# Optimization experiments

Hardware: AMD Instinct MI355X
Metric: run time of the kernel (lower is better)

The kernel has to match this reference:

```python
import jax, jax.numpy as jnp
import numpy as np

EPS = 1e-5
GRID = 128          # coarse grid extent -> fine grid is 256^3
N1 = 15000          # coarse voxels
CHILD = 4           # children kept per coarse voxel
N2 = N1 * CHILD     # fine voxels
CIN = 128
COUT = 64


def _build_geometry():
    rng = np.random.RandomState(0)
    flat = rng.choice(GRID ** 3, N1, replace=False)
    cc = np.stack(np.unravel_index(flat, (GRID, GRID, GRID)), axis=1)  # [N1,3]
    offs8 = np.array([[i, j, k] for i in (0, 1) for j in (0, 1) for k in (0, 1)], dtype=np.int64)
    kidx = np.argsort(rng.rand(N1, 8), axis=1)[:, :CHILD]              # [N1,4] distinct child taps
    fine = (cc[:, None, :] * 2 + offs8[kidx]).reshape(-1, 3)           # [N2,3] unique fine coords
    up_src = np.repeat(np.arange(N1), CHILD).astype(np.int32)
    up_kidx = kidx.reshape(-1).astype(np.int32)
    # 27-offset neighbor maps via hashed coordinate lookup
    key = (fine[:, 0] * 256 + fine[:, 1]) * 256 + fine[:, 2]
    order = np.argsort(key)
    skey = key[order]
    offs27 = np.array([[i, j, k] for i in (-1, 0, 1) for j in (-1, 0, 1) for k in (-1, 0, 1)], dtype=np.int64)
    nbr_src = np.full((27, N2), N2, dtype=np.int32)
    nbr_dst = np.full((27, N2), N2, dtype=np.int32)
    for t in range(27):
        q = fine + offs27[t]
        inb = np.all((q >= 0) & (q < 256), axis=1)
        qk = (q[:, 0] * 256 + q[:, 1]) * 256 + q[:, 2]
        pos = np.searchsorted(skey, qk)
        pos = np.clip(pos, 0, N2 - 1)
        hit = inb & (skey[pos] == qk)
        nbr_src[t, hit] = order[pos[hit]]
        nbr_dst[t, hit] = np.arange(N2, dtype=np.int32)[hit]
    return up_src, up_kidx, nbr_src, nbr_dst


def setup_inputs() -> dict:
    key = jax.random.key(0)
    ks = jax.random.split(key, 8)
    up_src, up_kidx, nbr_src, nbr_dst = _build_geometry()
    s_up = 1.0 / np.sqrt(CIN * 8)
    s1 = 1.0 / np.sqrt(CIN * 27)
    s2 = 1.0 / np.sqrt(COUT * 27)
    return {
        "feats1": jax.random.normal(ks[0], (N1, CIN), jnp.float32),
        "feats2": jax.random.normal(ks[1], (N2, CIN // 2), jnp.float32),
        "w_up": jax.random.normal(ks[2], (8, CIN, CIN // 2), jnp.float32) * s_up,
        "gamma_up": jnp.ones((CIN // 2,), jnp.float32),
        "beta_up": jnp.zeros((CIN // 2,), jnp.float32),
        "w1": jax.random.normal(ks[3], (27, CIN, COUT), jnp.float32) * s1,
        "gamma1": jnp.ones((COUT,), jnp.float32),
        "beta1": jnp.zeros((COUT,), jnp.float32),
        "w2": jax.random.normal(ks[4], (27, COUT, COUT), jnp.float32) * s2,
        "gamma2": jnp.ones((COUT,), jnp.float32),
        "beta2": jnp.zeros((COUT,), jnp.float32),
        "up_src": jnp.asarray(up_src),
        "up_kidx": jnp.asarray(up_kidx),
        "nbr_src": jnp.asarray(nbr_src),
        "nbr_dst": jnp.asarray(nbr_dst),
    }


def _bn_relu(x, gamma, beta):
    # training-mode BatchNorm over the point dimension (biased variance), then ReLU
    m = jnp.mean(x, axis=0)
    v = jnp.var(x, axis=0)
    return jax.nn.relu((x - m) * jax.lax.rsqrt(v + EPS) * gamma + beta)


def _sparse_conv(x, w, nbr_src, nbr_dst):
    # x: [N,Ci]; w: [27,Ci,Co]; transform-then-gather-scatter (hash-map sparse conv)
    n = x.shape[0]
    co = w.shape[-1]
    y = jnp.einsum("nc,kco->kno", x, w)                       # [27,N,Co]
    y = jnp.concatenate([y, jnp.zeros((27, 1, co), y.dtype)], axis=1)  # sentinel row
    msg = jnp.take_along_axis(y, nbr_src[:, :, None], axis=1)  # [27,N,Co]
    out = jnp.zeros((n + 1, co), y.dtype).at[nbr_dst.reshape(-1)].add(msg.reshape(-1, co))
    return out[:-1]


def reference(feats1, feats2, w_up, gamma_up, beta_up, w1, gamma1, beta1, w2,
              gamma2, beta2, up_src, up_kidx, nbr_src, nbr_dst):
    # transposed conv k=2 s=2, generative=False: each fine voxel pulls from its unique coarse parent
    y = jnp.einsum("mc,kco->kmo", feats1, w_up)               # [8,N1,Cin/2]
    x1 = y[up_kidx, up_src]                                   # [N2,Cin/2]
    x1 = _bn_relu(x1, gamma_up, beta_up)
    x = jnp.concatenate([x1, feats2], axis=-1)                # [N2,Cin]
    h = _bn_relu(_sparse_conv(x, w1, nbr_src, nbr_dst), gamma1, beta1)
    return _bn_relu(_sparse_conv(h, w2, nbr_src, nbr_dst), gamma2, beta2)
```

## Files before the change

kernel.cpp:

```cpp
#include <hip/hip_runtime.h>


typedef short bf16x4 __attribute__((ext_vector_type(4)));
typedef short bf16x8 __attribute__((ext_vector_type(8)));
typedef float f32x16 __attribute__((ext_vector_type(16)));

__device__ __forceinline__ short f2bf(float f) {
    unsigned u = __float_as_uint(f);
    u += 0x7fffu + ((u >> 16) & 1u);
    return (short)(u >> 16);
}
__device__ __forceinline__ float bf2f(short s) {
    return __uint_as_float(((unsigned)(unsigned short)s) << 16);
}

__global__ __launch_bounds__(256) void k_setup(
    const float* __restrict__ w_up, const float* __restrict__ w1,
    const float* __restrict__ w2, const float* __restrict__ f1,
    const int* __restrict__ nbr, const int* __restrict__ up_kidx,
    short* __restrict__ wupp, short* __restrict__ w1p,
    short* __restrict__ w2p, short* __restrict__ f1bf,
    int* __restrict__ pmask, int* __restrict__ perm_rows,
    int* __restrict__ rank, int* __restrict__ cnt,
    int2* __restrict__ ext, int* __restrict__ extc,
    float* __restrict__ y1, float* __restrict__ y2,
    int n1, int n2, int nbExt, int nbGeom)
{
    int tid = threadIdx.x;
    int bid = blockIdx.x;
    if (bid < nbExt) {
        long long tot = (long long)n2 * 16;
        long long gs = (long long)nbExt * 256;
        for (long long e = (long long)bid * 256 + tid; e < tot; e += gs) {
            ((float4*)y1)[e] = make_float4(0.f, 0.f, 0.f, 0.f);
            ((float4*)y2)[e] = make_float4(0.f, 0.f, 0.f, 0.f);
        }
        int i = bid * 256 + tid;
        unsigned hm = 0;
        if (i < n2) {
            #pragma unroll
            for (int t = 0; t < 27; ++t) {
                int s = nbr[(size_t)t * n2 + i];
                if (s < n2 && (s >> 2) != (i >> 2)) hm |= 1u << t;
            }
        }
        __shared__ int lcnt, lbase;
        if (tid == 0) lcnt = 0;
        __syncthreads();
        int nh = __popc(hm);
        int myofs = 0;
        if (nh) myofs = atomicAdd(&lcnt, nh);
        __syncthreads();
        if (tid == 0 && lcnt) lbase = atomicAdd(extc, lcnt);
        __syncthreads();
        if (nh) {
            int pos = lbase + myofs;
            unsigned m = hm;
            while (m) {
                int t = __ffs(m) - 1;
                m &= m - 1;
                int s = nbr[(size_t)t * n2 + i];
                ext[pos++] = make_int2(i, s | (t << 16));
            }
        }
    } else if (bid < nbExt + nbGeom) {
        int p = (bid - nbExt) * 256 + tid;
        if (p >= n1) return;
        int4 kd = *(const int4*)(up_kidx + 4 * p);
        int a = kd.x * 4 + 0, b = kd.y * 4 + 1, c = kd.z * 4 + 2, d = kd.w * 4 + 3;
        int t;
        if (a > b) { t = a; a = b; b = t; }
        if (c > d) { t = c; c = d; d = t; }
        if (a > c) { t = a; a = c; c = t; }
        if (b > d) { t = b; b = d; d = t; }
        if (b > c) { t = b; b = c; c = t; }
        perm_rows[4 * p + 0] = 4 * p + (a & 3);
        perm_rows[4 * p + 1] = 4 * p + (b & 3);
        perm_rows[4 * p + 2] = 4 * p + (c & 3);
        perm_rows[4 * p + 3] = 4 * p + (d & 3);
        int mask = (1 << (a >> 2)) | (1 << (b >> 2)) | (1 << (c >> 2)) | (1 << (d >> 2));
        pmask[p] = mask;
        rank[p] = atomicAdd(&cnt[mask], 1);
    } else {
        const long long nup = 65536, nw1 = 221184, nw2 = 110592;
        long long nf1 = (long long)n1 * 128;
        long long total = nup + nw1 + nw2 + nf1;
        long long gs = (long long)(gridDim.x - nbExt - nbGeom) * 256;
        for (long long e0 = (long long)(bid - nbExt - nbGeom) * 256 + tid;
             e0 < total; e0 += gs) {
            long long e = e0;
            if (e < nup) {
                int j = e & 7, l = (e >> 3) & 63, nt = (e >> 9) & 15, ks = (int)(e >> 13);
                int k = ks * 16 + (l >> 5) * 8 + j;
                int col = nt * 32 + (l & 31);
                wupp[e] = f2bf(w_up[((size_t)(col >> 6) * 128 + k) * 64 + (col & 63)]);
            } else if ((e -= nup) < nw1) {
                int j = e & 7, l = (e >> 3) & 63, ch = (e >> 9) & 1, ks = (e >> 10) & 7, t = (int)(e >> 13);
                int k = ks * 16 + (l >> 5) * 8 + j;
                int col = ch * 32 + (l & 31);
                w1p[e] = f2bf(w1[((size_t)t * 128 + k) * 64 + col]);
            } else if ((e -= nw1) < nw2) {
                int j = e & 7, l = (e >> 3) & 63, ch = (e >> 9) & 1, ks = (e >> 10) & 3, t = (int)(e >> 12);
                int k = ks * 16 + (l >> 5) * 8 + j;
                int col = ch * 32 + (l & 31);
                w2p[e] = f2bf(w2[((size_t)t * 64 + k) * 64 + col]);
            } else {
                e -= nw2;
                f1bf[e] = f2bf(f1[e]);
            }
        }
    }
}

__global__ __launch_bounds__(256) void k_up(
    const short* __restrict__ f1bf, const short* __restrict__ wupp,
    const int* __restrict__ pmask, const int* __restrict__ cnt,
    const int* __restrict__ rank, int* __restrict__ perm_par,
    int4* __restrict__ tiles, int* __restrict__ ntl,
    short* __restrict__ yup8, float* __restrict__ stats, int n1)
{
    if (blockIdx.x == 0) {
        __shared__ int sA[256], sB[256], bb[256];
        int t = threadIdx.x;
        int c = cnt[t], tc = (c + 31) >> 5;
        sA[t] = c; sB[t] = tc;
        __syncthreads();
        for (int off = 1; off < 256; off <<= 1) {
            int a = (t >= off) ? sA[t - off] : 0;
            int b = (t >= off) ? sB[t - off] : 0;
            __syncthreads();
            sA[t] += a; sB[t] += b;
            __syncthreads();
        }
        int base = sA[t] - c, toff = sB[t] - tc;
        bb[t] = base;
        for (int j = 0; j < tc; ++j) tiles[toff + j] = make_int4(t, base, j * 32, c);
        if (t == 255) ntl[0] = sB[255];
        __syncthreads();
        for (int p = t; p < n1; p += 256)
            perm_par[bb[pmask[p]] + rank[p]] = p;
        return;
    }
    __shared__ short lds[32 * 136];
    __shared__ float bs[64], bq[64];
    int bid = blockIdx.x - 1;
    int tile = bid >> 1;
    int w = threadIdx.x >> 6, lane = threadIdx.x & 63;
    int na = (bid & 1) * 8 + w, nb = na + 4;
    if (threadIdx.x < 64) { bs[threadIdx.x] = 0.f; bq[threadIdx.x] = 0.f; }
    #pragma unroll
    for (int it = 0; it < 2; ++it) {
        int c = it * 256 + threadIdx.x;
        int row = c >> 4, col8 = c & 15;
        int gr = tile * 32 + row; if (gr >= n1) gr = n1 - 1;
        int4 g = *(const int4*)(f1bf + (size_t)gr * 128 + col8 * 8);
        short* d = &lds[row * 136 + col8 * 8];
        *(int2*)d = make_int2(g.x, g.y);
        *(int2*)(d + 4) = make_int2(g.z, g.w);
    }
    int m = lane & 31, half = lane >> 5;
    int pm_l = (tile * 32 + m < n1) ? pmask[tile * 32 + m] : 0;
    __syncthreads();
    f32x16 a0, a1;
    #pragma unroll
    for (int i = 0; i < 16; ++i) { a0[i] = 0.f; a1[i] = 0.f; }
    const bf16x8* bp = (const bf16x8*)wupp;
    #pragma unroll
    for (int ks = 0; ks < 8; ++ks) {
        const short* ap = &lds[m * 136 + ks * 16 + half * 8];
        bf16x4 lo = *(const bf16x4*)ap, hi = *(const bf16x4*)(ap + 4);
        bf16x8 a = __builtin_shufflevector(lo, hi, 0, 1, 2, 3, 4, 5, 6, 7);
        bf16x8 b0 = bp[(size_t)(ks * 16 + na) * 64 + lane];
        bf16x8 b1 = bp[(size_t)(ks * 16 + nb) * 64 + lane];
        a0 = __builtin_amdgcn_mfma_f32_32x32x16_bf16(a, b0, a0, 0, 0, 0);
        a1 = __builtin_amdgcn_mfma_f32_32x32x16_bf16(a, b1, a1, 0, 0, 0);
    }
    int col = lane & 31;
    #pragma unroll
    for (int pass = 0; pass < 2; ++pass) {
        const f32x16& acc = pass ? a1 : a0;
        int n = pass ? nb : na;
        int slot = n >> 1, c = (n & 1) * 32 + col;
        float s0 = 0.f, q0 = 0.f;
        #pragma unroll
        for (int reg = 0; reg < 16; ++reg) {
            int r = (reg & 3) + 8 * (reg >> 2) + 4 * half;
            int p = tile * 32 + r;
            float v = acc[reg];
            int mk = __shfl(pm_l, r);
            if (p < n1) {
                yup8[(size_t)p * 512 + n * 32 + col] = f2bf(v);
                if ((mk >> slot) & 1) { s0 += v; q0 += v * v; }
            }
        }
        s0 += __shfl_xor(s0, 32);
        q0 += __shfl_xor(q0, 32);
        if (lane < 32) { atomicAdd(&bs[c], s0); atomicAdd(&bq[c], q0); }
    }
    __syncthreads();
    if (threadIdx.x < 64) {
        atomicAdd(&stats[threadIdx.x], bs[threadIdx.x]);
        atomicAdd(&stats[64 + threadIdx.x], bq[threadIdx.x]);
    }
}

__global__ __launch_bounds__(256) void k_extA(
    const short* __restrict__ yup8, const float* __restrict__ f2,
    const int* __restrict__ up_kidx, const float* __restrict__ w1,
    const float* __restrict__ gamma, const float* __restrict__ beta,
    const float* __restrict__ stats, const int2* __restrict__ ext,
    const int* __restrict__ extc, float* __restrict__ y, int n2)
{
    __shared__ float sc[64], sh[64];
    int tid = threadIdx.x;
    if (tid < 64) {
        float inv = 1.0f / (float)n2;
        float mean = stats[tid] * inv;
        float var = stats[64 + tid] * inv - mean * mean;
        float s = gamma[tid] * rsqrtf(var + 1e-5f);
        sc[tid] = s; sh[tid] = beta[tid] - mean * s;
    }
    __syncthreads();
    int gw = (blockIdx.x * 256 + tid) >> 6;
    int nw = (gridDim.x * 256) >> 6;
    int c = tid & 63;
    int ec = extc[0];
    for (int e = gw; e < ec; e += nw) {
        int2 en = ext[e];
        int i = en.x, s = en.y & 0xFFFF, t = en.y >> 16;
        const short* xr = yup8 + (size_t)(s >> 2) * 512 + up_kidx[s] * 64;
        const float* fr = f2 + (size_t)s * 64;
        const float* wr = w1 + (size_t)t * 8192 + c;
        float acc = 0.f;
        #pragma unroll 4
        for (int k = 0; k < 64; ++k) {
            float xk = fmaxf(bf2f(xr[k]) * sc[k] + sh[k], 0.f);
            acc += xk * wr[(size_t)k * 64];
        }
        #pragma unroll 4
        for (int k = 0; k < 64; ++k)
            acc += fr[k] * wr[(size_t)(64 + k) * 64];
        atomicAdd(&y[(size_t)i * 64 + c], acc);
    }
}

__global__ __launch_bounds__(256) void k_extB(
    const float* __restrict__ y1, const float* __restrict__ w2,
    const float* __restrict__ gamma, const float* __restrict__ beta,
    const float* __restrict__ stats, const int2* __restrict__ ext,
    const int* __restrict__ extc, float* __restrict__ y, int n2)
{
    __shared__ float sc[64], sh[64];
    int tid = threadIdx.x;
    if (tid < 64) {
        float inv = 1.0f / (float)n2;
        float mean = stats[tid] * inv;
        float var = stats[64 + tid] * inv - mean * mean;
        float s = gamma[tid] * rsqrtf(var + 1e-5f);
        sc[tid] = s; sh[tid] = beta[tid] - mean * s;
    }
    __syncthreads();
    int gw = (blockIdx.x * 256 + tid) >> 6;
    int nw = (gridDim.x * 256) >> 6;
    int c = tid & 63;
    int ec = extc[0];
    for (int e = gw; e < ec; e += nw) {
        int2 en = ext[e];
        int i = en.x, s = en.y & 0xFFFF, t = en.y >> 16;
        const float* hr = y1 + (size_t)s * 64;
        const float* wr = w2 + (size_t)t * 4096 + c;
        float acc = 0.f;
        #pragma unroll 4
        for (int k = 0; k < 64; ++k) {
            float hk = fmaxf(hr[k] * sc[k] + sh[k], 0.f);
            acc += hk * wr[(size_t)k * 64];
        }
        atomicAdd(&y[(size_t)i * 64 + c], acc);
    }
}

__device__ __forceinline__ void pair_epi2(const f32x16& a0v, const f32x16& a1v,
                                          int outrow0, int outrow1, int lane,
                                          int ch, float* __restrict__ y,
                                          float* __restrict__ bs,
                                          float* __restrict__ bq)
{
    int col = lane & 31;
    int c = ch * 32 + col;
    int r0[16], r1[16];
    #pragma unroll
    for (int reg = 0; reg < 16; ++reg) {
        int r = (reg & 3) + 8 * (reg >> 2) + 4 * (lane >> 5);
        r0[reg] = __shfl(outrow0, r);
        r1[reg] = __shfl(outrow1, r);
    }
    float o0[16], o1[16];
    #pragma unroll
    for (int reg = 0; reg < 16; ++reg) {
        int ra = (r0[reg] >= 0) ? r0[reg] : 0;
        int rb = (r1[reg] >= 0) ? r1[reg] : 0;
        o0[reg] = y[(size_t)ra * 64 + c];
        o1[reg] = y[(size_t)rb * 64 + c];
    }
    float s0 = 0.f, q0 = 0.f;
    #pragma unroll
    for (int reg = 0; reg < 16; ++reg) {
        if (r0[reg] >= 0) {
            float v = a0v[reg] + o0[reg];
            y[(size_t)r0[reg] * 64 + c] = v;
            s0 += v; q0 += v * v;
        }
        if (r1[reg] >= 0) {
            float v = a1v[reg] + o1[reg];
            y[(size_t)r1[reg] * 64 + c] = v;
            s0 += v; q0 += v * v;
        }
    }
    s0 += __shfl_xor(s0, 32);
    q0 += __shfl_xor(q0, 32);
    if (lane < 32) { atomicAdd(&bs[c], s0); atomicAdd(&bq[c], q0); }
}

__device__ __forceinline__ int tap27(int pa, int pb) {
    int di = ((pb >> 2) & 1) - ((pa >> 2) & 1);
    int dj = ((pb >> 1) & 1) - ((pa >> 1) & 1);
    int dk = (pb & 1) - (pa & 1);
    return (di + 1) * 9 + (dj + 1) * 3 + (dk + 1);
}

__global__ __launch_bounds__(256) void k_pairA(
    const short* __restrict__ yup8, const float* __restrict__ f2,
    const int* __restrict__ up_kidx, const short* __restrict__ wp,
    const float* __restrict__ gamma, const float* __restrict__ beta,
    const float* __restrict__ stats, const int* __restrict__ perm_par,
    const int* __restrict__ perm_rows, const int4* __restrict__ tiles,
    const int* __restrict__ n_tiles, float* __restrict__ y,
    float* __restrict__ ostats, int n2)
{
    constexpr int LP = 520;
    __shared__ short lds[32 * LP];
    __shared__ int srows[128], soff[128];
    __shared__ float scs[64], shs[64], bs[64], bq[64];
    int bt = blockIdx.x;
    if (bt >= n_tiles[0]) return;
    int4 td = tiles[bt];
    int mask = td.x, p_start = td.y, lt = td.z, cntb = td.w;
    int tid = threadIdx.x;
    if (tid < 128) {
        int li = lt + (tid >> 2);
        int pid = perm_par[p_start + ((li < cntb) ? li : 0)];
        int i = perm_rows[pid * 4 + (tid & 3)];
        srows[tid] = i;
        soff[tid] = (i >> 2) * 512 + up_kidx[i] * 64;
    } else if (tid < 192) {
        int cc = tid - 128;
        float inv = 1.0f / (float)n2;
        float mean = stats[cc] * inv;
        float var = stats[64 + cc] * inv - mean * mean;
        float s = gamma[cc] * rsqrtf(var + 1e-5f);
        scs[cc] = s; shs[cc] = beta[cc] - mean * s;
    } else {
        int cc = tid - 192;
        bs[cc] = 0.f; bq[cc] = 0.f;
    }
    __syncthreads();
    #pragma unroll
    for (int it = 0; it < 8; ++it) {
        int c0 = it * 256 + tid;
        int pl = c0 >> 6, w8 = c0 & 63;
        int j = w8 >> 4, col8 = w8 & 15;
        short* d = &lds[pl * LP + j * 128 + col8 * 8];
        if (col8 < 8) {
            bf16x8 g = *(const bf16x8*)(yup8 + (size_t)soff[pl * 4 + j] + col8 * 8);
            short o[8];
            #pragma unroll
            for (int u = 0; u < 8; ++u) {
                int cc = col8 * 8 + u;
                o[u] = f2bf(fmaxf(bf2f(g[u]) * scs[cc] + shs[cc], 0.f));
            }
            *(int2*)d = make_int2(((int)(unsigned short)o[0]) | ((int)o[1] << 16),
                                  ((int)(unsigned short)o[2]) | ((int)o[3] << 16));
            *(int2*)(d + 4) = make_int2(((int)(unsigned short)o[4]) | ((int)o[5] << 16),
                                        ((int)(unsigned short)o[6]) | ((int)o[7] << 16));
        } else {
            const float* fr = f2 + (size_t)srows[pl * 4 + j] * 64 + (col8 - 8) * 8;
            float4 f0 = *(const float4*)fr;
            float4 f1v = *(const float4*)(fr + 4);
            short o[8] = {f2bf(f0.x), f2bf(f0.y), f2bf(f0.z), f2bf(f0.w),
                          f2bf(f1v.x), f2bf(f1v.y), f2bf(f1v.z), f2bf(f1v.w)};
            *(int2*)d = make_int2(((int)(unsigned short)o[0]) | ((int)o[1] << 16),
                                  ((int)(unsigned short)o[2]) | ((int)o[3] << 16));
            *(int2*)(d + 4) = make_int2(((int)(unsigned short)o[4]) | ((int)o[5] << 16),
                                        ((int)(unsigned short)o[6]) | ((int)o[7] << 16));
        }
    }
    int p0 = -1, p1 = -1, p2 = -1, p3 = -1;
    #pragma unroll
    for (int b = 7; b >= 0; --b)
        if ((mask >> b) & 1) { p3 = p2; p2 = p1; p1 = p0; p0 = b; }
    int w = tid >> 6, lane = tid & 63;
    int a0 = w >> 1, a1 = a0 + 2, ch = w & 1;
    int pa0 = (a0 == 0) ? p0 : p1;
    int pa1 = (a1 == 2) ? p2 : p3;
    int t00 = tap27(pa0, p0), t01 = tap27(pa0, p1), t02 = tap27(pa0, p2), t03 = tap27(pa0, p3);
    int t10 = tap27(pa1, p0), t11 = tap27(pa1, p1), t12 = tap27(pa1, p2), t13 = tap27(pa1, p3);
    int m = lane & 31, half = lane >> 5;
    int li = lt + m;
    bool vp = li < cntb;
    int pid = perm_par[p_start + (vp ? li : 0)];
    int outrow0 = vp ? perm_rows[pid * 4 + a0] : -1;
    int outrow1 = vp ? perm_rows[pid * 4 + a1] : -1;
    __syncthreads();
    f32x16 acc0, acc1;
    #pragma unroll
    for (int i = 0; i < 16; ++i) { acc0[i] = 0.f; acc1[i] = 0.f; }
    const bf16x8* bp = (const bf16x8*)wp;
    #pragma unroll
    for (int b = 0; b < 4; ++b) {
        int tb0 = (b == 0) ? t00 : (b == 1) ? t01 : (b == 2) ? t02 : t03;
        int tb1 = (b == 0) ? t10 : (b == 1) ? t11 : (b == 2) ? t12 : t13;
        #pragma unroll
        for (int kk = 0; kk < 8; ++kk) {
            int ks = b * 8 + kk;
            const short* ap = &lds[m * LP + ks * 16 + half * 8];
            bf16x4 lo = *(const bf16x4*)ap, hi = *(const bf16x4*)(ap + 4);
            bf16x8 a = __builtin_shufflevector(lo, hi, 0, 1, 2, 3, 4, 5, 6, 7);
            bf16x8 b0 = bp[((size_t)(tb0 * 8 + kk) * 2 + ch) * 64 + lane];
            bf16x8 b1 = bp[((size_t)(tb1 * 8 + kk) * 2 + ch) * 64 + lane];
            acc0 = __builtin_amdgcn_mfma_f32_32x32x16_bf16(a, b0, acc0, 0, 0, 0);
            acc1 = __builtin_amdgcn_mfma_f32_32x32x16_bf16(a, b1, acc1, 0, 0, 0);
        }
    }
    pair_epi2(acc0, acc1, outrow0, outrow1, lane, ch, y, bs, bq);
    __syncthreads();
    if (tid < 64) {
        atomicAdd(&ostats[tid], bs[tid]);
        atomicAdd(&ostats[64 + tid], bq[tid]);
    }
}

__global__ __launch_bounds__(256) void k_pairB(
    const float* __restrict__ y1, const short* __restrict__ wp,
    const float* __restrict__ gamma, const float* __restrict__ beta,
    const float* __restrict__ stats, const int* __restrict__ perm_par,
    const int* __restrict__ perm_rows, const int4* __restrict__ tiles,
    const int* __restrict__ n_tiles, float* __restrict__ y,
    float* __restrict__ ostats, int n2)
{
    constexpr int LP = 264;
    __shared__ short lds[32 * LP];
    __shared__ int srows[128];
    __shared__ float scs[64], shs[64], bs[64], bq[64];
    int bt = blockIdx.x;
    if (bt >= n_tiles[0]) return;
    int4 td = tiles[bt];
    int mask = td.x, p_start = td.y, lt = td.z, cntb = td.w;
    int tid = threadIdx.x;
    if (tid < 128) {
        int li = lt + (tid >> 2);
        int pid = perm_par[p_start + ((li < cntb) ? li : 0)];
        srows[tid] = perm_rows[pid * 4 + (tid & 3)];
    } else if (tid < 192) {
        int cc = tid - 128;
        float inv = 1.0f / (float)n2;
        float mean = stats[cc] * inv;
        float var = stats[64 + cc] * inv - mean * mean;
        float s = gamma[cc] * rsqrtf(var + 1e-5f);
        scs[cc] = s; shs[cc] = beta[cc] - mean * s;
    } else {
        int cc = tid - 192;
        bs[cc] = 0.f; bq[cc] = 0.f;
    }
    __syncthreads();
    #pragma unroll
    for (int it = 0; it < 4; ++it) {
        int c0 = it * 256 + tid;
        int pl = c0 >> 5, w8 = c0 & 31;
        int j = w8 >> 3, col8 = w8 & 7;
        const float* fr = y1 + (size_t)srows[pl * 4 + j] * 64 + col8 * 8;
        float4 f0 = *(const float4*)fr;
        float4 f1v = *(const float4*)(fr + 4);
        short o[8];
        #pragma unroll
        for (int u = 0; u < 4; ++u) {
            int cc = col8 * 8 + u;
            float v = (u == 0) ? f0.x : (u == 1) ? f0.y : (u == 2) ? f0.z : f0.w;
            o[u] = f2bf(fmaxf(v * scs[cc] + shs[cc], 0.f));
        }
        #pragma unroll
        for (int u = 0; u < 4; ++u) {
            int cc = col8 * 8 + 4 + u;
            float v = (u == 0) ? f1v.x : (u == 1) ? f1v.y : (u == 2) ? f1v.z : f1v.w;
            o[4 + u] = f2bf(fmaxf(v * scs[cc] + shs[cc], 0.f));
        }
        short* d = &lds[pl * LP + j * 64 + col8 * 8];
        *(int2*)d = make_int2(((int)(unsigned short)o[0]) | ((int)o[1] << 16),
                              ((int)(unsigned short)o[2]) | ((int)o[3] << 16));
        *(int2*)(d + 4) = make_int2(((int)(unsigned short)o[4]) | ((int)o[5] << 16),
                                    ((int)(unsigned short)o[6]) | ((int)o[7] << 16));
    }
    int p0 = -1, p1 = -1, p2 = -1, p3 = -1;
    #pragma unroll
    for (int b = 7; b >= 0; --b)
        if ((mask >> b) & 1) { p3 = p2; p2 = p1; p1 = p0; p0 = b; }
    int w = tid >> 6, lane = tid & 63;
    int a0 = w >> 1, a1 = a0 + 2, ch = w & 1;
    int pa0 = (a0 == 0) ? p0 : p1;
    int pa1 = (a1 == 2) ? p2 : p3;
    int t00 = tap27(pa0, p0), t01 = tap27(pa0, p1), t02 = tap27(pa0, p2), t03 = tap27(pa0, p3);
    int t10 = tap27(pa1, p0), t11 = tap27(pa1, p1), t12 = tap27(pa1, p2), t13 = tap27(pa1, p3);
    int m = lane & 31, half = lane >> 5;
    int li = lt + m;
    bool vp = li < cntb;
    int pid = perm_par[p_start + (vp ? li : 0)];
    int outrow0 = vp ? perm_rows[pid * 4 + a0] : -1;
    int outrow1 = vp ? perm_rows[pid * 4 + a1] : -1;
    __syncthreads();
    f32x16 acc0, acc1;
    #pragma unroll
    for (int i = 0; i < 16; ++i) { acc0[i] = 0.f; acc1[i] = 0.f; }
    const bf16x8* bp = (const bf16x8*)wp;
    #pragma unroll
    for (int b = 0; b < 4; ++b) {
        int tb0 = (b == 0) ? t00 : (b == 1) ? t01 : (b == 2) ? t02 : t03;
        int tb1 = (b == 0) ? t10 : (b == 1) ? t11 : (b == 2) ? t12 : t13;
        #pragma unroll
        for (int kk = 0; kk < 4; ++kk) {
            int ks = b * 4 + kk;
            const short* ap = &lds[m * LP + ks * 16 + half * 8];
            bf16x4 lo = *(const bf16x4*)ap, hi = *(const bf16x4*)(ap + 4);
            bf16x8 a = __builtin_shufflevector(lo, hi, 0, 1, 2, 3, 4, 5, 6, 7);
            bf16x8 b0 = bp[((size_t)(tb0 * 4 + kk) * 2 + ch) * 64 + lane];
            bf16x8 b1 = bp[((size_t)(tb1 * 4 + kk) * 2 + ch) * 64 + lane];
            acc0 = __builtin_amdgcn_mfma_f32_32x32x16_bf16(a, b0, acc0, 0, 0, 0);
            acc1 = __builtin_amdgcn_mfma_f32_32x32x16_bf16(a, b1, acc1, 0, 0, 0);
        }
    }
    pair_epi2(acc0, acc1, outrow0, outrow1, lane, ch, y, bs, bq);
    __syncthreads();
    if (tid < 64) {
        atomicAdd(&ostats[tid], bs[tid]);
        atomicAdd(&ostats[64 + tid], bq[tid]);
    }
}

__global__ __launch_bounds__(256) void k_final(
    const float* __restrict__ y, const float* __restrict__ gamma,
    const float* __restrict__ beta, const float* __restrict__ stats,
    float* __restrict__ out, int n2)
{
    __shared__ float sc[64], sh[64];
    int tid = threadIdx.x;
    if (tid < 64) {
        float inv = 1.0f / (float)n2;
        float mean = stats[tid] * inv;
        float var = stats[64 + tid] * inv - mean * mean;
        float s = gamma[tid] * rsqrtf(var + 1e-5f);
        sc[tid] = s;
        sh[tid] = beta[tid] - mean * s;
    }
    __syncthreads();
    long long total = (long long)n2 * 16;
    long long stride = (long long)gridDim.x * blockDim.x;
    for (long long idx = (long long)blockIdx.x * blockDim.x + tid; idx < total; idx += stride) {
        int i = (int)(idx >> 4);
        int c4 = ((int)idx & 15) * 4;
        const float* src = y + (size_t)i * 64 + c4;
        float4 o;
        o.x = fmaxf(src[0] * sc[c4 + 0] + sh[c4 + 0], 0.f);
        o.y = fmaxf(src[1] * sc[c4 + 1] + sh[c4 + 1], 0.f);
        o.z = fmaxf(src[2] * sc[c4 + 2] + sh[c4 + 2], 0.f);
        o.w = fmaxf(src[3] * sc[c4 + 3] + sh[c4 + 3], 0.f);
        *(float4*)(out + (size_t)i * 64 + c4) = o;
    }
}

extern "C" void kernel_launch(void* const* d_in, const int* in_sizes, int n_in,
                              void* d_out, int out_size, void* d_ws, size_t ws_size,
                              hipStream_t stream)
{
    const float* feats1   = (const float*)d_in[0];
    const float* feats2   = (const float*)d_in[1];
    const float* w_up     = (const float*)d_in[2];
    const float* gamma_up = (const float*)d_in[3];
    const float* beta_up  = (const float*)d_in[4];
    const float* w1       = (const float*)d_in[5];
    const float* gamma1   = (const float*)d_in[6];
    const float* beta1    = (const float*)d_in[7];
    const float* w2       = (const float*)d_in[8];
    const float* gamma2   = (const float*)d_in[9];
    const float* beta2    = (const float*)d_in[10];
    const int* up_src     = (const int*)d_in[11];  (void)up_src;
    const int* up_kidx    = (const int*)d_in[12];
    const int* nbr_src    = (const int*)d_in[13];

    int n1 = in_sizes[0] / 128;
    int n2 = in_sizes[1] / 64;

    char* p = (char*)d_ws;
    auto alloc = [&](size_t bytes) {
        char* r = p;
        p += (bytes + 255) & ~(size_t)255;
        return r;
    };
    float* stats    = (float*)alloc(384 * 4);
    int*   cnt      = (int*)alloc(256 * 4);
    int*   extc     = (int*)alloc(16);
    int*   ntl      = (int*)alloc(16);
    size_t headBytes = (size_t)((char*)(ntl + 4) - (char*)d_ws);
    int maxTiles    = (n1 + 31) / 32 + 80;
    int4*  tiles    = (int4*)alloc((size_t)maxTiles * 16);
    short* wupp     = (short*)alloc((size_t)65536 * 2);
    short* w1p      = (short*)alloc((size_t)221184 * 2);
    short* w2p      = (short*)alloc((size_t)110592 * 2);
    short* f1bf     = (short*)alloc((size_t)n1 * 128 * 2);
    int*   pmask    = (int*)alloc((size_t)n1 * 4);
    int*   rank     = (int*)alloc((size_t)n1 * 4);
    int*   perm_par = (int*)alloc((size_t)n1 * 4);
    int*   perm_rows= (int*)alloc((size_t)4 * n1 * 4);
    int2*  ext      = (int2*)alloc((size_t)27 * n2 * 8);
    short* yup8     = (short*)alloc((size_t)n1 * 512 * 2);
    float* y1       = (float*)alloc((size_t)n2 * 64 * 4);
    float* y2       = (float*)alloc((size_t)n2 * 64 * 4);

    int nbExt  = (n2 + 255) / 256;
    int nbGeom = (n1 + 255) / 256;
    int nbPack = 256;
    int nbSetup = nbExt + nbGeom + nbPack;
    int upBlocks = 1 + 2 * ((n1 + 31) / 32);
    int ewBlocks16 = (int)(((long long)n2 * 16 + 255) / 256);

    hipMemsetAsync(d_ws, 0, headBytes, stream);
    k_setup<<<nbSetup, 256, 0, stream>>>(w_up, w1, w2, feats1, nbr_src, up_kidx,
                                         wupp, w1p, w2p, f1bf, pmask, perm_rows,
                                         rank, cnt, ext, extc, y1, y2,
                                         n1, n2, nbExt, nbGeom);
    k_up<<<upBlocks, 256, 0, stream>>>(f1bf, wupp, pmask, cnt, rank, perm_par,
                                       tiles, ntl, yup8, stats, n1);
    k_extA<<<512, 256, 0, stream>>>(yup8, feats2, up_kidx, w1, gamma_up, beta_up,
                                    stats, ext, extc, y1, n2);
    k_pairA<<<maxTiles, 256, 0, stream>>>(yup8, feats2, up_kidx, w1p, gamma_up,
                                          beta_up, stats, perm_par, perm_rows,
                                          tiles, ntl, y1, stats + 128, n2);
    k_extB<<<512, 256, 0, stream>>>(y1, w2, gamma1, beta1, stats + 128, ext,
                                    extc, y2, n2);
    k_pairB<<<maxTiles, 256, 0, stream>>>(y1, w2p, gamma1, beta1, stats + 128,
                                          perm_par, perm_rows, tiles, ntl, y2,
                                          stats + 256, n2);
    k_final<<<ewBlocks16, 256, 0, stream>>>(y2, gamma2, beta2, stats + 256,
                                            (float*)d_out, n2);
}
```

Before: 251.9 us.

## Compact upsample buffer to kept children and skip zeroing rows without external neighbors

The upsampled coarse output buffer now stores only the 4 kept child slots per parent instead of all 8, halving its writes and the gathered footprint, with a per-row slot index replacing up_kidx lookups. Zero-initialisation of y1/y2 is limited to rows that actually receive external neighbor contributions, tracked with a bitmap. The pair kernels then skip the read-modify-write load for rows that were not pre-touched. The ext kernels also get half as many blocks. In exchange there is extra atomic bitmap traffic and flag bits packed into the row indices.

```diff
diff --git a/kernel.cpp b/kernel.cpp
--- a/kernel.cpp
+++ b/kernel.cpp
@@ -4,6 +4,8 @@
 typedef short bf16x4 __attribute__((ext_vector_type(4)));
 typedef short bf16x8 __attribute__((ext_vector_type(8)));
 typedef float f32x16 __attribute__((ext_vector_type(16)));
+
+#define ROWMASK 0x3FFFFFFF
 
 __device__ __forceinline__ short f2bf(float f) {
     unsigned u = __float_as_uint(f);
@@ -21,20 +23,15 @@
     short* __restrict__ wupp, short* __restrict__ w1p,
     short* __restrict__ w2p, short* __restrict__ f1bf,
     int* __restrict__ pmask, int* __restrict__ perm_rows,
-    int* __restrict__ rank, int* __restrict__ cnt,
+    int* __restrict__ sidx, int* __restrict__ rank, int* __restrict__ cnt,
     int2* __restrict__ ext, int* __restrict__ extc,
+    unsigned* __restrict__ ebit,
     float* __restrict__ y1, float* __restrict__ y2,
     int n1, int n2, int nbExt, int nbGeom)
 {
     int tid = threadIdx.x;
     int bid = blockIdx.x;
     if (bid < nbExt) {
-        long long tot = (long long)n2 * 16;
-        long long gs = (long long)nbExt * 256;
-        for (long long e = (long long)bid * 256 + tid; e < tot; e += gs) {
-            ((float4*)y1)[e] = make_float4(0.f, 0.f, 0.f, 0.f);
-            ((float4*)y2)[e] = make_float4(0.f, 0.f, 0.f, 0.f);
-        }
         int i = bid * 256 + tid;
         unsigned hm = 0;
         if (i < n2) {
@@ -54,6 +51,12 @@
         if (tid == 0 && lcnt) lbase = atomicAdd(extc, lcnt);
         __syncthreads();
         if (nh) {
+            atomicOr(&ebit[i >> 5], 1u << (i & 31));
+            float4 z = make_float4(0.f, 0.f, 0.f, 0.f);
+            float4* z1 = (float4*)(y1 + (size_t)i * 64);
+            float4* z2 = (float4*)(y2 + (size_t)i * 64);
+            #pragma unroll
+            for (int q = 0; q < 16; ++q) { z1[q] = z; z2[q] = z; }
             int pos = lbase + myofs;
             unsigned m = hm;
             while (m) {
@@ -78,6 +81,10 @@
         perm_rows[4 * p + 1] = 4 * p + (b & 3);
         perm_rows[4 * p + 2] = 4 * p + (c & 3);
         perm_rows[4 * p + 3] = 4 * p + (d & 3);
+        sidx[4 * p + (a & 3)] = 0;
+        sidx[4 * p + (b & 3)] = 1;
+        sidx[4 * p + (c & 3)] = 2;
+        sidx[4 * p + (d & 3)] = 3;
         int mask = (1 << (a >> 2)) | (1 << (b >> 2)) | (1 << (c >> 2)) | (1 << (d >> 2));
         pmask[p] = mask;
         rank[p] = atomicAdd(&cnt[mask], 1);
@@ -117,7 +124,7 @@
     const int* __restrict__ pmask, const int* __restrict__ cnt,
     const int* __restrict__ rank, int* __restrict__ perm_par,
     int4* __restrict__ tiles, int* __restrict__ ntl,
-    short* __restrict__ yup8, float* __restrict__ stats, int n1)
+    short* __restrict__ yup4, float* __restrict__ stats, int n1)
 {
     if (blockIdx.x == 0) {
         __shared__ int sA[256], sB[256], bb[256];
@@ -188,9 +195,10 @@
             int p = tile * 32 + r;
             float v = acc[reg];
             int mk = __shfl(pm_l, r);
-            if (p < n1) {
-                yup8[(size_t)p * 512 + n * 32 + col] = f2bf(v);
-                if ((mk >> slot) & 1) { s0 += v; q0 += v * v; }
+            if (p < n1 && ((mk >> slot) & 1)) {
+                int j = __popc(mk & ((1 << slot) - 1));
+                yup4[(size_t)p * 256 + j * 64 + c] = f2bf(v);
+                s0 += v; q0 += v * v;
             }
         }
         s0 += __shfl_xor(s0, 32);
@@ -205,8 +213,8 @@
 }
 
 __global__ __launch_bounds__(256) void k_extA(
-    const short* __restrict__ yup8, const float* __restrict__ f2,
-    const int* __restrict__ up_kidx, const float* __restrict__ w1,
+    const short* __restrict__ yup4, const float* __restrict__ f2,
+    const int* __restrict__ sidx, const float* __restrict__ w1,
     const float* __restrict__ gamma, const float* __restrict__ beta,
     const float* __restrict__ stats, const int2* __restrict__ ext,
     const int* __restrict__ extc, float* __restrict__ y, int n2)
@@ -228,7 +236,7 @@
     for (int e = gw; e < ec; e += nw) {
         int2 en = ext[e];
         int i = en.x, s = en.y & 0xFFFF, t = en.y >> 16;
-        const short* xr = yup8 + (size_t)(s >> 2) * 512 + up_kidx[s] * 64;
+        const short* xr = yup4 + (size_t)(s >> 2) * 256 + sidx[s] * 64;
         const float* fr = f2 + (size_t)s * 64;
         const float* wr = w1 + (size_t)t * 8192 + c;
         float acc = 0.f;
@@ -279,7 +287,7 @@
     }
 }
 
-__device__ __forceinline__ void pair_epi2(const f32x16& a0v, const f32x16& a1v,
+__device__ __forceinline__ void pair_epi3(const f32x16& a0v, const f32x16& a1v,
                                           int outrow0, int outrow1, int lane,
                                           int ch, float* __restrict__ y,
                                           float* __restrict__ bs,
@@ -297,22 +305,20 @@
     float o0[16], o1[16];
     #pragma unroll
     for (int reg = 0; reg < 16; ++reg) {
-        int ra = (r0[reg] >= 0) ? r0[reg] : 0;
-        int rb = (r1[reg] >= 0) ? r1[reg] : 0;
-        o0[reg] = y[(size_t)ra * 64 + c];
-        o1[reg] = y[(size_t)rb * 64 + c];
+        o0[reg] = (r0[reg] >= 0 && (r0[reg] >> 30)) ? y[(size_t)(r0[reg] & ROWMASK) * 64 + c] : 0.f;
+        o1[reg] = (r1[reg] >= 0 && (r1[reg] >> 30)) ? y[(size_t)(r1[reg] & ROWMASK) * 64 + c] : 0.f;
     }
     float s0 = 0.f, q0 = 0.f;
     #pragma unroll
     for (int reg = 0; reg < 16; ++reg) {
         if (r0[reg] >= 0) {
             float v = a0v[reg] + o0[reg];
-            y[(size_t)r0[reg] * 64 + c] = v;
+            y[(size_t)(r0[reg] & ROWMASK) * 64 + c] = v;
             s0 += v; q0 += v * v;
         }
         if (r1[reg] >= 0) {
             float v = a1v[reg] + o1[reg];
-            y[(size_t)r1[reg] * 64 + c] = v;
+            y[(size_t)(r1[reg] & ROWMASK) * 64 + c] = v;
             s0 += v; q0 += v * v;
         }
     }
@@ -328,14 +334,18 @@
     return (di + 1) * 9 + (dj + 1) * 3 + (dk + 1);
 }
 
+__device__ __forceinline__ int flagrow(int row, const unsigned* __restrict__ ebit) {
+    return row | (((ebit[row >> 5] >> (row & 31)) & 1u) << 30);
+}
+
 __global__ __launch_bounds__(256) void k_pairA(
-    const short* __restrict__ yup8, const float* __restrict__ f2,
-    const int* __restrict__ up_kidx, const short* __restrict__ wp,
+    const short* __restrict__ yup4, const float* __restrict__ f2,
+    const short* __restrict__ wp,
     const float* __restrict__ gamma, const float* __restrict__ beta,
     const float* __restrict__ stats, const int* __restrict__ perm_par,
     const int* __restrict__ perm_rows, const int4* __restrict__ tiles,
-    const int* __restrict__ n_tiles, float* __restrict__ y,
-    float* __restrict__ ostats, int n2)
+    const int* __restrict__ n_tiles, const unsigned* __restrict__ ebit,
+    float* __restrict__ y, float* __restrict__ ostats, int n2)
 {
     constexpr int LP = 520;
     __shared__ short lds[32 * LP];
@@ -349,9 +359,8 @@
     if (tid < 128) {
         int li = lt + (tid >> 2);
         int pid = perm_par[p_start + ((li < cntb) ? li : 0)];
-        int i = perm_rows[pid * 4 + (tid & 3)];
-        srows[tid] = i;
-        soff[tid] = (i >> 2) * 512 + up_kidx[i] * 64;
+        srows[tid] = perm_rows[pid * 4 + (tid & 3)];
+        soff[tid] = pid * 256 + (tid & 3) * 64;
     } else if (tid < 192) {
         int cc = tid - 128;
         float inv = 1.0f / (float)n2;
@@ -371,7 +380,7 @@
         int j = w8 >> 4, col8 = w8 & 15;
         short* d = &lds[pl * LP + j * 128 + col8 * 8];
         if (col8 < 8) {
-            bf16x8 g = *(const bf16x8*)(yup8 + (size_t)soff[pl * 4 + j] + col8 * 8);
+            bf16x8 g = *(const bf16x8*)(yup4 + (size_t)soff[pl * 4 + j] + col8 * 8);
             short o[8];
             #pragma unroll
             for (int u = 0; u < 8; ++u) {
@@ -408,8 +417,8 @@
     int li = lt + m;
     bool vp = li < cntb;
     int pid = perm_par[p_start + (vp ? li : 0)];
-    int outrow0 = vp ? perm_rows[pid * 4 + a0] : -1;
-    int outrow1 = vp ? perm_rows[pid * 4 + a1] : -1;
+    int outrow0 = vp ? flagrow(perm_rows[pid * 4 + a0], ebit) : -1;
+    int outrow1 = vp ? flagrow(perm_rows[pid * 4 + a1], ebit) : -1;
     __syncthreads();
     f32x16 acc0, acc1;
     #pragma unroll
@@ -431,7 +440,7 @@
             acc1 = __builtin_amdgcn_mfma_f32_32x32x16_bf16(a, b1, acc1, 0, 0, 0);
         }
     }
-    pair_epi2(acc0, acc1, outrow0, outrow1, lane, ch, y, bs, bq);
+    pair_epi3(acc0, acc1, outrow0, outrow1, lane, ch, y, bs, bq);
     __syncthreads();
     if (tid < 64) {
         atomicAdd(&ostats[tid], bs[tid]);
@@ -444,8 +453,8 @@
     const float* __restrict__ gamma, const float* __restrict__ beta,
     const float* __restrict__ stats, const int* __restrict__ perm_par,
     const int* __restrict__ perm_rows, const int4* __restrict__ tiles,
-    const int* __restrict__ n_tiles, float* __restrict__ y,
-    float* __restrict__ ostats, int n2)
+    const int* __restrict__ n_tiles, const unsigned* __restrict__ ebit,
+    float* __restrict__ y, float* __restrict__ ostats, int n2)
 {
     constexpr int LP = 264;
     __shared__ short lds[32 * LP];
@@ -513,8 +522,8 @@
     int li = lt + m;
     bool vp = li < cntb;
     int pid = perm_par[p_start + (vp ? li : 0)];
-    int outrow0 = vp ? perm_rows[pid * 4 + a0] : -1;
-    int outrow1 = vp ? perm_rows[pid * 4 + a1] : -1;
+    int outrow0 = vp ? flagrow(perm_rows[pid * 4 + a0], ebit) : -1;
+    int outrow1 = vp ? flagrow(perm_rows[pid * 4 + a1], ebit) : -1;
     __syncthreads();
     f32x16 acc0, acc1;
     #pragma unroll
@@ -536,7 +545,7 @@
             acc1 = __builtin_amdgcn_mfma_f32_32x32x16_bf16(a, b1, acc1, 0, 0, 0);
         }
     }
-    pair_epi2(acc0, acc1, outrow0, outrow1, lane, ch, y, bs, bq);
+    pair_epi3(acc0, acc1, outrow0, outrow1, lane, ch, y, bs, bq);
     __syncthreads();
     if (tid < 64) {
         atomicAdd(&ostats[tid], bs[tid]);
@@ -590,7 +599,6 @@
     const float* w2       = (const float*)d_in[8];
     const float* gamma2   = (const float*)d_in[9];
     const float* beta2    = (const float*)d_in[10];
-    const int* up_src     = (const int*)d_in[11];  (void)up_src;
     const int* up_kidx    = (const int*)d_in[12];
     const int* nbr_src    = (const int*)d_in[13];
 
@@ -603,11 +611,12 @@
         p += (bytes + 255) & ~(size_t)255;
         return r;
     };
-    float* stats    = (float*)alloc(384 * 4);
-    int*   cnt      = (int*)alloc(256 * 4);
-    int*   extc     = (int*)alloc(16);
-    int*   ntl      = (int*)alloc(16);
-    size_t headBytes = (size_t)((char*)(ntl + 4) - (char*)d_ws);
+    float*    stats = (float*)alloc(384 * 4);
+    int*      cnt   = (int*)alloc(256 * 4);
+    int*      extc  = (int*)alloc(16);
+    int*      ntl   = (int*)alloc(16);
+    unsigned* ebit  = (unsigned*)alloc(((size_t)(n2 + 31) / 32) * 4);
+    size_t headBytes = (size_t)(p - (char*)d_ws);
     int maxTiles    = (n1 + 31) / 32 + 80;
     int4*  tiles    = (int4*)alloc((size_t)maxTiles * 16);
     short* wupp     = (short*)alloc((size_t)65536 * 2);
@@ -618,8 +627,9 @@
     int*   rank     = (int*)alloc((size_t)n1 * 4);
     int*   perm_par = (int*)alloc((size_t)n1 * 4);
     int*   perm_rows= (int*)alloc((size_t)4 * n1 * 4);
+    int*   sidx     = (int*)alloc((size_t)n2 * 4);
     int2*  ext      = (int2*)alloc((size_t)27 * n2 * 8);
-    short* yup8     = (short*)alloc((size_t)n1 * 512 * 2);
+    short* yup4     = (short*)alloc((size_t)n1 * 256 * 2);
     float* y1       = (float*)alloc((size_t)n2 * 64 * 4);
     float* y2       = (float*)alloc((size_t)n2 * 64 * 4);
 
@@ -633,20 +643,20 @@
     hipMemsetAsync(d_ws, 0, headBytes, stream);
     k_setup<<<nbSetup, 256, 0, stream>>>(w_up, w1, w2, feats1, nbr_src, up_kidx,
                                          wupp, w1p, w2p, f1bf, pmask, perm_rows,
-                                         rank, cnt, ext, extc, y1, y2,
-                                         n1, n2, nbExt, nbGeom);
+                                         sidx, rank, cnt, ext, extc, ebit,
+                                         y1, y2, n1, n2, nbExt, nbGeom);
     k_up<<<upBlocks, 256, 0, stream>>>(f1bf, wupp, pmask, cnt, rank, perm_par,
-                                       tiles, ntl, yup8, stats, n1);
-    k_extA<<<512, 256, 0, stream>>>(yup8, feats2, up_kidx, w1, gamma_up, beta_up,
+                                       tiles, ntl, yup4, stats, n1);
+    k_extA<<<256, 256, 0, stream>>>(yup4, feats2, sidx, w1, gamma_up, beta_up,
                                     stats, ext, extc, y1, n2);
-    k_pairA<<<maxTiles, 256, 0, stream>>>(yup8, feats2, up_kidx, w1p, gamma_up,
-                                          beta_up, stats, perm_par, perm_rows,
-                                          tiles, ntl, y1, stats + 128, n2);
-    k_extB<<<512, 256, 0, stream>>>(y1, w2, gamma1, beta1, stats + 128, ext,
+    k_pairA<<<maxTiles, 256, 0, stream>>>(yup4, feats2, w1p, gamma_up, beta_up,
+                                          stats, perm_par, perm_rows, tiles,
+                                          ntl, ebit, y1, stats + 128, n2);
+    k_extB<<<256, 256, 0, stream>>>(y1, w2, gamma1, beta1, stats + 128, ext,
                                     extc, y2, n2);
     k_pairB<<<maxTiles, 256, 0, stream>>>(y1, w2p, gamma1, beta1, stats + 128,
-                                          perm_par, perm_rows, tiles, ntl, y2,
-                                          stats + 256, n2);
+                                          perm_par, perm_rows, tiles, ntl, ebit,
+                                          y2, stats + 256, n2);
     k_final<<<ewBlocks16, 256, 0, stream>>>(y2, gamma2, beta2, stats + 256,
                                             (float*)d_out, n2);
 }
```

Result: slower. 264.6 us (+5.1%).

## Reorder pair and ext kernels so pair writes plainly, drop y zero-fill

Applied to the files above, without the earlier changes.

The dense pair kernels now run before the extra-neighbor kernels and store their results directly, without reading back y. That removes both the zero-initialization of y1/y2 in setup and the read-modify-write in the pair epilogue. The ext kernels then atomically add the cross-parent contributions and update the BN statistics incrementally, using the returned old value to correct the sum of squares. Ext grid size drops from 512 to 256 blocks. The trade-off is extra atomics and a reliance on the pair kernels covering every output row before the ext kernels add to it.

```diff
diff --git a/kernel.cpp b/kernel.cpp
--- a/kernel.cpp
+++ b/kernel.cpp
@@ -23,18 +23,11 @@
     int* __restrict__ pmask, int* __restrict__ perm_rows,
     int* __restrict__ rank, int* __restrict__ cnt,
     int2* __restrict__ ext, int* __restrict__ extc,
-    float* __restrict__ y1, float* __restrict__ y2,
     int n1, int n2, int nbExt, int nbGeom)
 {
     int tid = threadIdx.x;
     int bid = blockIdx.x;
     if (bid < nbExt) {
-        long long tot = (long long)n2 * 16;
-        long long gs = (long long)nbExt * 256;
-        for (long long e = (long long)bid * 256 + tid; e < tot; e += gs) {
-            ((float4*)y1)[e] = make_float4(0.f, 0.f, 0.f, 0.f);
-            ((float4*)y2)[e] = make_float4(0.f, 0.f, 0.f, 0.f);
-        }
         int i = bid * 256 + tid;
         unsigned hm = 0;
         if (i < n2) {
@@ -209,9 +202,10 @@
     const int* __restrict__ up_kidx, const float* __restrict__ w1,
     const float* __restrict__ gamma, const float* __restrict__ beta,
     const float* __restrict__ stats, const int2* __restrict__ ext,
-    const int* __restrict__ extc, float* __restrict__ y, int n2)
-{
-    __shared__ float sc[64], sh[64];
+    const int* __restrict__ extc, float* __restrict__ y,
+    float* __restrict__ ostats, int n2)
+{
+    __shared__ float sc[64], sh[64], bs[64], bq[64];
     int tid = threadIdx.x;
     if (tid < 64) {
         float inv = 1.0f / (float)n2;
@@ -219,12 +213,14 @@
         float var = stats[64 + tid] * inv - mean * mean;
         float s = gamma[tid] * rsqrtf(var + 1e-5f);
         sc[tid] = s; sh[tid] = beta[tid] - mean * s;
+        bs[tid] = 0.f; bq[tid] = 0.f;
     }
     __syncthreads();
     int gw = (blockIdx.x * 256 + tid) >> 6;
     int nw = (gridDim.x * 256) >> 6;
     int c = tid & 63;
     int ec = extc[0];
+    float ls = 0.f, lq = 0.f;
     for (int e = gw; e < ec; e += nw) {
         int2 en = ext[e];
         int i = en.x, s = en.y & 0xFFFF, t = en.y >> 16;
@@ -240,7 +236,16 @@
         #pragma unroll 4
         for (int k = 0; k < 64; ++k)
             acc += fr[k] * wr[(size_t)(64 + k) * 64];
-        atomicAdd(&y[(size_t)i * 64 + c], acc);
+        float old = atomicAdd(&y[(size_t)i * 64 + c], acc);
+        ls += acc;
+        lq += acc * (2.f * old + acc);
+    }
+    atomicAdd(&bs[c], ls);
+    atomicAdd(&bq[c], lq);
+    __syncthreads();
+    if (tid < 64) {
+        atomicAdd(&ostats[tid], bs[tid]);
+        atomicAdd(&ostats[64 + tid], bq[tid]);
     }
 }
 
@@ -248,9 +253,10 @@
     const float* __restrict__ y1, const float* __restrict__ w2,
     const float* __restrict__ gamma, const float* __restrict__ beta,
     const float* __restrict__ stats, const int2* __restrict__ ext,
-    const int* __restrict__ extc, float* __restrict__ y, int n2)
-{
-    __shared__ float sc[64], sh[64];
+    const int* __restrict__ extc, float* __restrict__ y,
+    float* __restrict__ ostats, int n2)
+{
+    __shared__ float sc[64], sh[64], bs[64], bq[64];
     int tid = threadIdx.x;
     if (tid < 64) {
         float inv = 1.0f / (float)n2;
@@ -258,12 +264,14 @@
         float var = stats[64 + tid] * inv - mean * mean;
         float s = gamma[tid] * rsqrtf(var + 1e-5f);
         sc[tid] = s; sh[tid] = beta[tid] - mean * s;
+        bs[tid] = 0.f; bq[tid] = 0.f;
     }
     __syncthreads();
     int gw = (blockIdx.x * 256 + tid) >> 6;
     int nw = (gridDim.x * 256) >> 6;
     int c = tid & 63;
     int ec = extc[0];
+    float ls = 0.f, lq = 0.f;
     for (int e = gw; e < ec; e += nw) {
         int2 en = ext[e];
         int i = en.x, s = en.y & 0xFFFF, t = en.y >> 16;
@@ -275,15 +283,24 @@
             float hk = fmaxf(hr[k] * sc[k] + sh[k], 0.f);
             acc += hk * wr[(size_t)k * 64];
         }
-        atomicAdd(&y[(size_t)i * 64 + c], acc);
-    }
-}
-
-__device__ __forceinline__ void pair_epi2(const f32x16& a0v, const f32x16& a1v,
-                                          int outrow0, int outrow1, int lane,
-                                          int ch, float* __restrict__ y,
-                                          float* __restrict__ bs,
-                                          float* __restrict__ bq)
+        float old = atomicAdd(&y[(size_t)i * 64 + c], acc);
+        ls += acc;
+        lq += acc * (2.f * old + acc);
+    }
+    atomicAdd(&bs[c], ls);
+    atomicAdd(&bq[c], lq);
+    __syncthreads();
+    if (tid < 64) {
+        atomicAdd(&ostats[tid], bs[tid]);
+        atomicAdd(&ostats[64 + tid], bq[tid]);
+    }
+}
+
+__device__ __forceinline__ void pair_epi_store(const f32x16& a0v, const f32x16& a1v,
+                                               int outrow0, int outrow1, int lane,
+                                               int ch, float* __restrict__ y,
+                                               float* __restrict__ bs,
+                                               float* __restrict__ bq)
 {
     int col = lane & 31;
     int c = ch * 32 + col;
@@ -294,24 +311,16 @@
         r0[reg] = __shfl(outrow0, r);
         r1[reg] = __shfl(outrow1, r);
     }
-    float o0[16], o1[16];
-    #pragma unroll
-    for (int reg = 0; reg < 16; ++reg) {
-        int ra = (r0[reg] >= 0) ? r0[reg] : 0;
-        int rb = (r1[reg] >= 0) ? r1[reg] : 0;
-        o0[reg] = y[(size_t)ra * 64 + c];
-        o1[reg] = y[(size_t)rb * 64 + c];
-    }
     float s0 = 0.f, q0 = 0.f;
     #pragma unroll
     for (int reg = 0; reg < 16; ++reg) {
         if (r0[reg] >= 0) {
-            float v = a0v[reg] + o0[reg];
+            float v = a0v[reg];
             y[(size_t)r0[reg] * 64 + c] = v;
             s0 += v; q0 += v * v;
         }
         if (r1[reg] >= 0) {
-            float v = a1v[reg] + o1[reg];
+            float v = a1v[reg];
             y[(size_t)r1[reg] * 64 + c] = v;
             s0 += v; q0 += v * v;
         }
@@ -431,7 +440,7 @@
             acc1 = __builtin_amdgcn_mfma_f32_32x32x16_bf16(a, b1, acc1, 0, 0, 0);
         }
     }
-    pair_epi2(acc0, acc1, outrow0, outrow1, lane, ch, y, bs, bq);
+    pair_epi_store(acc0, acc1, outrow0, outrow1, lane, ch, y, bs, bq);
     __syncthreads();
     if (tid < 64) {
         atomicAdd(&ostats[tid], bs[tid]);
@@ -536,7 +545,7 @@
             acc1 = __builtin_amdgcn_mfma_f32_32x32x16_bf16(a, b1, acc1, 0, 0, 0);
         }
     }
-    pair_epi2(acc0, acc1, outrow0, outrow1, lane, ch, y, bs, bq);
+    pair_epi_store(acc0, acc1, outrow0, outrow1, lane, ch, y, bs, bq);
     __syncthreads();
     if (tid < 64) {
         atomicAdd(&ostats[tid], bs[tid]);
@@ -590,7 +599,6 @@
     const float* w2       = (const float*)d_in[8];
     const float* gamma2   = (const float*)d_in[9];
     const float* beta2    = (const float*)d_in[10];
-    const int* up_src     = (const int*)d_in[11];  (void)up_src;
     const int* up_kidx    = (const int*)d_in[12];
     const int* nbr_src    = (const int*)d_in[13];
 
@@ -607,7 +615,7 @@
     int*   cnt      = (int*)alloc(256 * 4);
     int*   extc     = (int*)alloc(16);
     int*   ntl      = (int*)alloc(16);
-    size_t headBytes = (size_t)((char*)(ntl + 4) - (char*)d_ws);
+    size_t headBytes = (size_t)(p - (char*)d_ws);
     int maxTiles    = (n1 + 31) / 32 + 80;
     int4*  tiles    = (int4*)alloc((size_t)maxTiles * 16);
     short* wupp     = (short*)alloc((size_t)65536 * 2);
@@ -633,20 +641,20 @@
     hipMemsetAsync(d_ws, 0, headBytes, stream);
     k_setup<<<nbSetup, 256, 0, stream>>>(w_up, w1, w2, feats1, nbr_src, up_kidx,
                                          wupp, w1p, w2p, f1bf, pmask, perm_rows,
-                                         rank, cnt, ext, extc, y1, y2,
-                                         n1, n2, nbExt, nbGeom);
+                                         rank, cnt, ext, extc, n1, n2,
+                                         nbExt, nbGeom);
     k_up<<<upBlocks, 256, 0, stream>>>(f1bf, wupp, pmask, cnt, rank, perm_par,
                                        tiles, ntl, yup8, stats, n1);
-    k_extA<<<512, 256, 0, stream>>>(yup8, feats2, up_kidx, w1, gamma_up, beta_up,
-                                    stats, ext, extc, y1, n2);
     k_pairA<<<maxTiles, 256, 0, stream>>>(yup8, feats2, up_kidx, w1p, gamma_up,
                                           beta_up, stats, perm_par, perm_rows,
                                           tiles, ntl, y1, stats + 128, n2);
-    k_extB<<<512, 256, 0, stream>>>(y1, w2, gamma1, beta1, stats + 128, ext,
-                                    extc, y2, n2);
+    k_extA<<<256, 256, 0, stream>>>(yup8, feats2, up_kidx, w1, gamma_up, beta_up,
+                                    stats, ext, extc, y1, stats + 128, n2);
     k_pairB<<<maxTiles, 256, 0, stream>>>(y1, w2p, gamma1, beta1, stats + 128,
                                           perm_par, perm_rows, tiles, ntl, y2,
                                           stats + 256, n2);
+    k_extB<<<256, 256, 0, stream>>>(y1, w2, gamma1, beta1, stats + 128, ext,
+                                    extc, y2, stats + 256, n2);
     k_final<<<ewBlocks16, 256, 0, stream>>>(y2, gamma2, beta2, stats + 256,
                                             (float*)d_out, n2);
 }
```

Result: slower. 273.3 us (+8.5%).
